# Optimization experiments

Hardware: AMD Instinct MI355X
Metric: run time of the kernel (lower is better)

## Reference

```python
import jax, jax.numpy as jnp
import numpy as np

C0 = 32          # cs[0] == cs[1] with planes=[32,32,...], cr=1.0
CIN = 4
EPS = 1e-5

# ---------- host-side coordinate hashing (mirrors F.sphash / F.sphashquery) ----------

def _enc(c):
    # unique int64 code per (x,y,z); +2 shift keeps offset-adjusted coords positive
    return (c[:, 0] + 2).astype(np.int64) + (c[:, 1] + 2).astype(np.int64) * 1024 \
        + (c[:, 2] + 2).astype(np.int64) * 1024 * 1024

def _lookup(sorted_codes, q):
    pos = np.searchsorted(sorted_codes, q)
    pos = np.minimum(pos, len(sorted_codes) - 1)
    return np.where(sorted_codes[pos] == q, pos, -1).astype(np.int32)

def _offsets(r):
    return np.array([[i, j, k] for i in r for j in r for k in r], np.int64)


def setup_inputs() -> dict:
    rng = np.random.default_rng(0)
    N0 = 400000
    pts = rng.integers(0, [400, 400, 40], size=(600000, 3)).astype(np.int64)
    codes = _enc(pts)
    codes_u, idx = np.unique(codes, return_index=True)
    assert len(codes_u) >= N0
    coords0, codes0 = pts[idx][:N0], codes_u[:N0]   # sorted by hash code

    off27, off8 = _offsets([-1, 0, 1]), _offsets([0, 1])
    # ks=3 stride=1 kernel map at level 0: nbr0[k, i] = index of coords0[i]+off27[k] (or -1)
    nbr0 = np.stack([_lookup(codes0, _enc(coords0 + o)) for o in off27])

    # stride-2 downsample coords (level 1)
    c1all = coords0 // 2
    codes1_u, i1 = np.unique(_enc(c1all), return_index=True)
    coords1 = c1all[i1]
    # ks=2 stride=2 kernel map: output voxel gathers inputs at 2*out + {0,1}^3
    down1 = np.stack([_lookup(codes0, _enc(coords1 * 2 + o)) for o in off8])
    # ks=3 stride=1 kernel map at level 1
    nbr1 = np.stack([_lookup(codes1_u, _enc(coords1 + o)) for o in off27])

    key = jax.random.key(0)
    ks = jax.random.split(key, 10)

    def w(k, K, ci, co):
        return jax.random.normal(k, (K, ci, co), jnp.float32) * (1.0 / np.sqrt(K * ci))

    return {
        "voxel_features": jax.random.normal(ks[0], (N0, CIN), jnp.float32),
        "W_stem1": w(ks[1], 27, CIN, C0),
        "W_stem2": w(ks[2], 27, C0, C0),
        "W_down":  w(ks[3], 8,  C0, C0),
        "W_r1a":   w(ks[4], 27, C0, C0),
        "W_r1b":   w(ks[5], 27, C0, C0),
        "W_r2a":   w(ks[6], 27, C0, C0),
        "W_r2b":   w(ks[7], 27, C0, C0),
        "gammas": jnp.ones((7, C0), jnp.float32),
        "betas":  jnp.zeros((7, C0), jnp.float32),
        "nbr0":  jnp.asarray(nbr0),
        "down1": jnp.asarray(down1),
        "nbr1":  jnp.asarray(nbr1),
    }


# ---------- sparse conv: gather-GEMM-scatter per kernel offset ----------

def _spconv(feat, nbr, W):
    # feat [N, Ci], nbr [K, M] (-1 = no neighbor), W [K, Ci, Co] -> out [M, Co]
    def step(acc, kw):
        idx, Wk = kw
        g = jnp.where((idx >= 0)[:, None], feat[jnp.maximum(idx, 0)], 0.0)
        return acc + g @ Wk, None
    acc0 = jnp.zeros((nbr.shape[1], W.shape[-1]), feat.dtype)
    out, _ = jax.lax.scan(step, acc0, (nbr, W))
    return out


def _bn(x, g, b):
    # BatchNorm1d, training-mode statistics (biased var), gamma/beta affine
    mu = x.mean(0)
    var = x.var(0)
    return (x - mu) * jax.lax.rsqrt(var + EPS) * g + b


def _cbr(x, nbr, W, g, b):
    return jax.nn.relu(_bn(_spconv(x, nbr, W), g, b))


def reference(voxel_features, W_stem1, W_stem2, W_down, W_r1a, W_r1b, W_r2a, W_r2b,
              gammas, betas, nbr0, down1, nbr1):
    g, b = gammas, betas
    # stem: two ks=3 sparse convs + BN + ReLU at level 0
    x = _cbr(voxel_features, nbr0, W_stem1, g[0], b[0])
    x = _cbr(x, nbr0, W_stem2, g[1], b[1])
    # stage1: BasicConvolutionBlock (ks=2, stride=2) + 2 ResidualBlocks at level 1
    x1 = _cbr(x, down1, W_down, g[2], b[2])
    h = _cbr(x1, nbr1, W_r1a, g[3], b[3])
    h = _bn(_spconv(h, nbr1, W_r1b), g[4], b[4])
    x1 = jax.nn.relu(h + x1)          # downsample == Identity (inc == outc, stride 1)
    h = _cbr(x1, nbr1, W_r2a, g[5], b[5])
    h = _bn(_spconv(h, nbr1, W_r2b), g[6], b[6])
    return jax.nn.relu(h + x1)
```

## Files before the change

kernel.cpp:

```cpp
#include <hip/hip_runtime.h>

#define EPS 1e-5f

typedef __attribute__((ext_vector_type(8))) short short8;
typedef __attribute__((ext_vector_type(4))) float floatx4;
typedef __attribute__((ext_vector_type(8))) unsigned short ushort8;
typedef __attribute__((ext_vector_type(4))) unsigned short ushortv4;

#define O_S1  0
#define O_S2  4096
#define O_DN  (O_S2 + 27648)
#define O_R1A (O_DN + 8192)
#define O_R1B (O_R1A + 27648)
#define O_R2A (O_R1B + 27648)
#define O_R2B (O_R2A + 27648)
#define WP_TOTAL (O_R2B + 27648)

__device__ __forceinline__ unsigned short f2bf(float f) {
    union { float f; unsigned u; } x; x.f = f;
    unsigned r = x.u + 0x7fffu + ((x.u >> 16) & 1u);
    return (unsigned short)(r >> 16);
}
__device__ __forceinline__ float bf2f(unsigned short b) {
    union { unsigned u; float f; } x; x.u = ((unsigned)b) << 16;
    return x.f;
}

__device__ __forceinline__ int xcd_swizzle(int nb) {
    int b = (int)blockIdx.x;
    int q = nb >> 3, r = nb & 7;
    int x = b & 7, i = b >> 3;
    return x * q + (x < r ? x : r) + i;
}

__device__ __forceinline__ short8 gath(const unsigned short* __restrict__ x,
                                       int ii, int q) {
    short8 z = {};
    return (ii >= 0) ? *(const short8*)(x + (size_t)ii * 32 + q * 8) : z;
}

__device__ __forceinline__ void pack_w_one(
    const float* __restrict__ W, unsigned short* __restrict__ out, int t)
{
    int lane = t & 63;
    int h = (t >> 6) & 1;
    int k = t >> 7;
    int m = lane & 15, q = lane >> 4;
    ushort8 v;
#pragma unroll
    for (int j = 0; j < 8; ++j)
        v[j] = f2bf(W[((size_t)k * 32 + q * 8 + j) * 32 + h * 16 + m]);
    *(ushort8*)(out + (size_t)t * 8) = v;
}

__global__ __launch_bounds__(256) void prep_kernel(
    const float* __restrict__ vf,
    const float* __restrict__ Ws1, const float* __restrict__ Ws2,
    const float* __restrict__ Wd,  const float* __restrict__ Wr1a,
    const float* __restrict__ Wr1b, const float* __restrict__ Wr2a,
    const float* __restrict__ Wr2b,
    unsigned short* __restrict__ xb, unsigned short* __restrict__ wp, int N0)
{
    int t = blockIdx.x * 256 + threadIdx.x;
    if (t < N0) {
        float4 v = *(const float4*)(vf + (size_t)t * 4);
        ushortv4 r = {f2bf(v.x), f2bf(v.y), f2bf(v.z), f2bf(v.w)};
        *(ushortv4*)(xb + (size_t)t * 4) = r;
        return;
    }
    t -= N0;
    if (t < 512) {
        int lane = t & 63;
        int h = (t >> 6) & 1;
        int c = t >> 7;
        int m = lane & 15, q = lane >> 4;
        ushort8 v;
#pragma unroll
        for (int j = 0; j < 8; ++j) {
            int kdim = c * 32 + q * 8 + j;
            int tap = kdim >> 2, ci = kdim & 3;
            v[j] = (tap < 27) ? f2bf(Ws1[((size_t)tap * 4 + ci) * 32 + h * 16 + m]) : 0;
        }
        *(ushort8*)(wp + O_S1 + (size_t)t * 8) = v;
        return;
    }
    t -= 512;
    if (t < 27 * 128) { pack_w_one(Ws2,  wp + O_S2,  t); return; }
    t -= 27 * 128;
    if (t < 8 * 128)  { pack_w_one(Wd,   wp + O_DN,  t); return; }
    t -= 8 * 128;
    if (t < 27 * 128) { pack_w_one(Wr1a, wp + O_R1A, t); return; }
    t -= 27 * 128;
    if (t < 27 * 128) { pack_w_one(Wr1b, wp + O_R1B, t); return; }
    t -= 27 * 128;
    if (t < 27 * 128) { pack_w_one(Wr2a, wp + O_R2A, t); return; }
    t -= 27 * 128;
    if (t < 27 * 128) { pack_w_one(Wr2b, wp + O_R2B, t); return; }
}

__device__ __forceinline__ void conv_epilogue2(
    floatx4 acc00, floatx4 acc01, floatx4 acc10, floatx4 acc11,
    unsigned short* __restrict__ y, float* __restrict__ part,
    int rowbase, int lb, int N, float* sm)
{
    const int lane = threadIdx.x & 63;
    const int m = lane & 15, q = lane >> 4;

    if (threadIdx.x < 64) sm[threadIdx.x] = 0.f;
    __syncthreads();

#pragma unroll
    for (int r = 0; r < 4; ++r) {
        int ra = rowbase + q * 4 + r;
        int rb = ra + 16;
        if (ra < N) {
            y[(size_t)ra * 32 + m]      = f2bf(acc00[r]);
            y[(size_t)ra * 32 + 16 + m] = f2bf(acc01[r]);
        }
        if (rb < N) {
            y[(size_t)rb * 32 + m]      = f2bf(acc10[r]);
            y[(size_t)rb * 32 + 16 + m] = f2bf(acc11[r]);
        }
    }

    float s0 = 0.f, q0 = 0.f, s1 = 0.f, q1 = 0.f;
#pragma unroll
    for (int r = 0; r < 4; ++r) {
        s0 += acc00[r] + acc10[r];
        q0 += acc00[r] * acc00[r] + acc10[r] * acc10[r];
        s1 += acc01[r] + acc11[r];
        q1 += acc01[r] * acc01[r] + acc11[r] * acc11[r];
    }
    s0 += __shfl_down(s0, 32); s0 += __shfl_down(s0, 16);
    q0 += __shfl_down(q0, 32); q0 += __shfl_down(q0, 16);
    s1 += __shfl_down(s1, 32); s1 += __shfl_down(s1, 16);
    q1 += __shfl_down(q1, 32); q1 += __shfl_down(q1, 16);
    if (lane < 16) {
        atomicAdd(&sm[m],      s0);
        atomicAdd(&sm[32 + m], q0);
        atomicAdd(&sm[16 + m],      s1);
        atomicAdd(&sm[48 + m], q1);
    }
    __syncthreads();
    if (threadIdx.x < 64)
        part[(size_t)lb * 64 + threadIdx.x] = sm[threadIdx.x];
}

#define MFMA_BF16 __builtin_amdgcn_mfma_f32_16x16x32_bf16
template <int K>
__global__ __launch_bounds__(256) void conv_mfma_kernel(
    const unsigned short* __restrict__ x,
    const int* __restrict__ nbr,
    const unsigned short* __restrict__ Wp,
    unsigned short* __restrict__ y,
    float* __restrict__ part, int N)
{
    __shared__ float sm[64];
    const int nb = (N + 255) / 256;
    const int lb = xcd_swizzle(nb);
    const int lane = threadIdx.x & 63;
    const int wave = threadIdx.x >> 6;
    const int m = lane & 15, q = lane >> 4;
    const int rowbase = lb * 256 + wave * 64;
    const int r0 = rowbase + m, r1 = r0 + 16, r2 = r0 + 32, r3 = r0 + 48;
    const bool v0 = r0 < N, v1 = r1 < N, v2 = r2 < N, v3 = r3 < N;

    floatx4 c00 = {0.f, 0.f, 0.f, 0.f};
    floatx4 c01 = c00, c10 = c00, c11 = c00;
    floatx4 c20 = c00, c21 = c00, c30 = c00, c31 = c00;

#define IDX(k, rr, vv) ((vv) ? nbr[(size_t)(k) * N + (rr)] : -1)

    int p0 = IDX(0, r0, v0), p1 = IDX(0, r1, v1), p2 = IDX(0, r2, v2), p3 = IDX(0, r3, v3);
    short8 a0 = gath(x, p0, q), a1 = gath(x, p1, q), a2 = gath(x, p2, q), a3 = gath(x, p3, q);
    int j0 = -1, j1 = -1, j2 = -1, j3 = -1;
    if (K > 1) { j0 = IDX(1, r0, v0); j1 = IDX(1, r1, v1); j2 = IDX(1, r2, v2); j3 = IDX(1, r3, v3); }

    for (int k = 0; k < K; ++k) {
        int n0 = -1, n1 = -1, n2 = -1, n3 = -1;
        if (k + 2 < K) {
            n0 = IDX(k + 2, r0, v0); n1 = IDX(k + 2, r1, v1);
            n2 = IDX(k + 2, r2, v2); n3 = IDX(k + 2, r3, v3);
        }
        short8 t0 = {}, t1 = {}, t2 = {}, t3 = {};
        if (k + 1 < K) {
            t0 = gath(x, j0, q); t1 = gath(x, j1, q);
            t2 = gath(x, j2, q); t3 = gath(x, j3, q);
        }
        const short8* wk = (const short8*)(Wp + (size_t)k * 1024);
        short8 b0 = wk[lane];
        short8 b1 = wk[64 + lane];
        c00 = MFMA_BF16(a0, b0, c00, 0, 0, 0);
        c01 = MFMA_BF16(a0, b1, c01, 0, 0, 0);
        c10 = MFMA_BF16(a1, b0, c10, 0, 0, 0);
        c11 = MFMA_BF16(a1, b1, c11, 0, 0, 0);
        c20 = MFMA_BF16(a2, b0, c20, 0, 0, 0);
        c21 = MFMA_BF16(a2, b1, c21, 0, 0, 0);
        c30 = MFMA_BF16(a3, b0, c30, 0, 0, 0);
        c31 = MFMA_BF16(a3, b1, c31, 0, 0, 0);
        a0 = t0; a1 = t1; a2 = t2; a3 = t3;
        j0 = n0; j1 = n1; j2 = n2; j3 = n3;
    }
#undef IDX

    if (threadIdx.x < 64) sm[threadIdx.x] = 0.f;
    __syncthreads();

#define STORE2(cA, cB, tb)                                        \
    _Pragma("unroll")                                             \
    for (int r = 0; r < 4; ++r) {                                 \
        int ra = rowbase + (tb) * 16 + q * 4 + r;                 \
        if (ra < N) {                                             \
            y[(size_t)ra * 32 + m]      = f2bf(cA[r]);            \
            y[(size_t)ra * 32 + 16 + m] = f2bf(cB[r]);            \
        }                                                         \
    }
    STORE2(c00, c01, 0) STORE2(c10, c11, 1) STORE2(c20, c21, 2) STORE2(c30, c31, 3)
#undef STORE2

    float s0 = 0.f, q0 = 0.f, s1 = 0.f, q1 = 0.f;
#pragma unroll
    for (int r = 0; r < 4; ++r) {
        s0 += c00[r] + c10[r] + c20[r] + c30[r];
        q0 += c00[r] * c00[r] + c10[r] * c10[r] + c20[r] * c20[r] + c30[r] * c30[r];
        s1 += c01[r] + c11[r] + c21[r] + c31[r];
        q1 += c01[r] * c01[r] + c11[r] * c11[r] + c21[r] * c21[r] + c31[r] * c31[r];
    }
    s0 += __shfl_down(s0, 32); s0 += __shfl_down(s0, 16);
    q0 += __shfl_down(q0, 32); q0 += __shfl_down(q0, 16);
    s1 += __shfl_down(s1, 32); s1 += __shfl_down(s1, 16);
    q1 += __shfl_down(q1, 32); q1 += __shfl_down(q1, 16);
    if (lane < 16) {
        atomicAdd(&sm[m],      s0);
        atomicAdd(&sm[32 + m], q0);
        atomicAdd(&sm[16 + m],      s1);
        atomicAdd(&sm[48 + m], q1);
    }
    __syncthreads();
    if (threadIdx.x < 64)
        part[(size_t)lb * 64 + threadIdx.x] = sm[threadIdx.x];
}

__global__ __launch_bounds__(256) void conv_stem1_mfma(
    const unsigned short* __restrict__ xb,
    const int* __restrict__ nbr,
    const unsigned short* __restrict__ Wp,
    unsigned short* __restrict__ y,
    float* __restrict__ part, int N)
{
    __shared__ float sm[64];
    const int nb = (N + 127) / 128;
    const int lb = xcd_swizzle(nb);
    const int lane = threadIdx.x & 63;
    const int wave = threadIdx.x >> 6;
    const int m = lane & 15, q = lane >> 4;
    const int rowbase = lb * 128 + wave * 32;
    const int row0 = rowbase + m;
    const int row1 = rowbase + 16 + m;

    floatx4 acc00 = {0.f, 0.f, 0.f, 0.f};
    floatx4 acc01 = acc00, acc10 = acc00, acc11 = acc00;

#pragma unroll
    for (int c = 0; c < 4; ++c) {
        const int t0 = c * 8 + q * 2, t1 = t0 + 1;
        short8 a0 = {}, a1 = {};
        {
            int ia = (t0 < 27 && row0 < N) ? nbr[(size_t)t0 * N + row0] : -1;
            int ib = (t1 < 27 && row0 < N) ? nbr[(size_t)t1 * N + row0] : -1;
            ushortv4 ga = {}, gb = {};
            if (ia >= 0) ga = *(const ushortv4*)(xb + (size_t)ia * 4);
            if (ib >= 0) gb = *(const ushortv4*)(xb + (size_t)ib * 4);
            a0[0] = (short)ga[0]; a0[1] = (short)ga[1];
            a0[2] = (short)ga[2]; a0[3] = (short)ga[3];
            a0[4] = (short)gb[0]; a0[5] = (short)gb[1];
            a0[6] = (short)gb[2]; a0[7] = (short)gb[3];
        }
        {
            int ia = (t0 < 27 && row1 < N) ? nbr[(size_t)t0 * N + row1] : -1;
            int ib = (t1 < 27 && row1 < N) ? nbr[(size_t)t1 * N + row1] : -1;
            ushortv4 ga = {}, gb = {};
            if (ia >= 0) ga = *(const ushortv4*)(xb + (size_t)ia * 4);
            if (ib >= 0) gb = *(const ushortv4*)(xb + (size_t)ib * 4);
            a1[0] = (short)ga[0]; a1[1] = (short)ga[1];
            a1[2] = (short)ga[2]; a1[3] = (short)ga[3];
            a1[4] = (short)gb[0]; a1[5] = (short)gb[1];
            a1[6] = (short)gb[2]; a1[7] = (short)gb[3];
        }
        const short8* wk = (const short8*)Wp;
        short8 b0 = wk[(c * 2 + 0) * 64 + lane];
        short8 b1 = wk[(c * 2 + 1) * 64 + lane];
        acc00 = MFMA_BF16(a0, b0, acc00, 0, 0, 0);
        acc01 = MFMA_BF16(a0, b1, acc01, 0, 0, 0);
        acc10 = MFMA_BF16(a1, b0, acc10, 0, 0, 0);
        acc11 = MFMA_BF16(a1, b1, acc11, 0, 0, 0);
    }

    conv_epilogue2(acc00, acc01, acc10, acc11, y, part, rowbase, lb, N, sm);
}

__global__ __launch_bounds__(256) void reduce_stats_kernel(
    const float* __restrict__ part, float* __restrict__ stats, int nb)
{
    __shared__ float sm[256];
    int t = threadIdx.x;
    int c = t & 63, g = t >> 6;
    float s = 0.f;
    for (int b = blockIdx.x * 4 + g; b < nb; b += 256)
        s += part[(size_t)b * 64 + c];
    sm[t] = s;
    __syncthreads();
    if (t < 64)
        atomicAdd(&stats[t], sm[t] + sm[64 + t] + sm[128 + t] + sm[192 + t]);
}

template <bool OUT_F32, bool HAS_RES>
__global__ __launch_bounds__(256) void bn_relu_kernel(
    const unsigned short* __restrict__ y, const float* __restrict__ stats,
    const float* __restrict__ gamma, const float* __restrict__ beta,
    const unsigned short* __restrict__ resid, void* __restrict__ outp, int N)
{
    int t = blockIdx.x * 256 + threadIdx.x;
    if (t >= N) return;
    float inv_n = 1.0f / (float)N;
    const ushort8* yr = (const ushort8*)(y + (size_t)t * 32);

#pragma unroll
    for (int c = 0; c < 4; ++c) {
        ushort8 v = yr[c];
        ushort8 rv = {};
        if (HAS_RES) rv = ((const ushort8*)(resid + (size_t)t * 32))[c];
        float f0, f1, f2, f3, f4, f5, f6, f7;
#define BNJ(fj, j)                                                        \
        {                                                                 \
            int co = c * 8 + (j);                                         \
            float mu = stats[co] * inv_n;                                 \
            float var = stats[32 + co] * inv_n - mu * mu;                 \
            float sc = rsqrtf(var + EPS) * gamma[co];                     \
            fj = (bf2f(v[j]) - mu) * sc + beta[co];                       \
            if (HAS_RES) fj += bf2f(rv[j]);                               \
            fj = fmaxf(fj, 0.0f);                                         \
        }
        BNJ(f0, 0) BNJ(f1, 1) BNJ(f2, 2) BNJ(f3, 3)
        BNJ(f4, 4) BNJ(f5, 5) BNJ(f6, 6) BNJ(f7, 7)
#undef BNJ
        if (OUT_F32) {
            float* ob = (float*)outp + (size_t)t * 32 + c * 8;
            floatx4 u0 = {f0, f1, f2, f3}, u1 = {f4, f5, f6, f7};
            *(floatx4*)(ob) = u0;
            *(floatx4*)(ob + 4) = u1;
        } else {
            ushort8 o;
            o[0] = f2bf(f0); o[1] = f2bf(f1); o[2] = f2bf(f2); o[3] = f2bf(f3);
            o[4] = f2bf(f4); o[5] = f2bf(f5); o[6] = f2bf(f6); o[7] = f2bf(f7);
            ((ushort8*)((unsigned short*)outp + (size_t)t * 32))[c] = o;
        }
    }
}

extern "C" void kernel_launch(void* const* d_in, const int* in_sizes, int n_in,
                              void* d_out, int out_size, void* d_ws, size_t ws_size,
                              hipStream_t stream)
{
    const float* vf   = (const float*)d_in[0];
    const float* Ws1  = (const float*)d_in[1];
    const float* Ws2  = (const float*)d_in[2];
    const float* Wd   = (const float*)d_in[3];
    const float* Wr1a = (const float*)d_in[4];
    const float* Wr1b = (const float*)d_in[5];
    const float* Wr2a = (const float*)d_in[6];
    const float* Wr2b = (const float*)d_in[7];
    const float* gam  = (const float*)d_in[8];
    const float* bet  = (const float*)d_in[9];
    const int* nbr0   = (const int*)d_in[10];
    const int* down1  = (const int*)d_in[11];
    const int* nbr1   = (const int*)d_in[12];

    int N0 = in_sizes[0] / 4;
    int N1 = in_sizes[11] / 8;

    unsigned short* yraw = (unsigned short*)d_ws;
    unsigned short* actA = yraw + (size_t)N0 * 32;
    unsigned short* actB = actA + (size_t)N0 * 32;
    unsigned short* xb   = actB + (size_t)N0 * 32;
    unsigned short* wp   = xb + (size_t)N0 * 4;
    float* part  = (float*)(wp + WP_TOTAL);
    float* stats = part + (size_t)3200 * 64;

    hipMemsetAsync(stats, 0, 7 * 64 * sizeof(float), stream);

    auto g1 = [](int n) { return dim3((unsigned)((n + 255) / 256)); };
    auto gm = [](int n) { return dim3((unsigned)((n + 255) / 256)); };
    auto gs = [](int n) { return dim3((unsigned)((n + 127) / 128)); };
    int nbs1 = (N0 + 127) / 128;
    int nb0 = (N0 + 255) / 256;
    int nb1 = (N1 + 255) / 256;

    int prep_threads = N0 + 512 + 128 * (27 * 5 + 8);
    prep_kernel<<<g1(prep_threads), 256, 0, stream>>>(
        vf, Ws1, Ws2, Wd, Wr1a, Wr1b, Wr2a, Wr2b, xb, wp, N0);

    conv_stem1_mfma<<<gs(N0), 256, 0, stream>>>(xb, nbr0, wp + O_S1, yraw, part, N0);
    reduce_stats_kernel<<<64, 256, 0, stream>>>(part, stats + 0 * 64, nbs1);
    bn_relu_kernel<false, false><<<g1(N0), 256, 0, stream>>>(yraw, stats + 0 * 64, gam + 0, bet + 0, nullptr, actA, N0);
    conv_mfma_kernel<27><<<gm(N0), 256, 0, stream>>>(actA, nbr0, wp + O_S2, yraw, part, N0);
    reduce_stats_kernel<<<64, 256, 0, stream>>>(part, stats + 1 * 64, nb0);
    bn_relu_kernel<false, false><<<g1(N0), 256, 0, stream>>>(yraw, stats + 1 * 64, gam + 32, bet + 32, nullptr, actB, N0);
    conv_mfma_kernel<8><<<gm(N1), 256, 0, stream>>>(actB, down1, wp + O_DN, yraw, part, N1);
    reduce_stats_kernel<<<64, 256, 0, stream>>>(part, stats + 2 * 64, nb1);
    bn_relu_kernel<false, false><<<g1(N1), 256, 0, stream>>>(yraw, stats + 2 * 64, gam + 64, bet + 64, nullptr, actA, N1);
    conv_mfma_kernel<27><<<gm(N1), 256, 0, stream>>>(actA, nbr1, wp + O_R1A, yraw, part, N1);
    reduce_stats_kernel<<<64, 256, 0, stream>>>(part, stats + 3 * 64, nb1);
    bn_relu_kernel<false, false><<<g1(N1), 256, 0, stream>>>(yraw, stats + 3 * 64, gam + 96, bet + 96, nullptr, actB, N1);
    conv_mfma_kernel<27><<<gm(N1), 256, 0, stream>>>(actB, nbr1, wp + O_R1B, yraw, part, N1);
    reduce_stats_kernel<<<64, 256, 0, stream>>>(part, stats + 4 * 64, nb1);
    bn_relu_kernel<false, true><<<g1(N1), 256, 0, stream>>>(yraw, stats + 4 * 64, gam + 128, bet + 128, actA, actB, N1);
    conv_mfma_kernel<27><<<gm(N1), 256, 0, stream>>>(actB, nbr1, wp + O_R2A, yraw, part, N1);
    reduce_stats_kernel<<<64, 256, 0, stream>>>(part, stats + 5 * 64, nb1);
    bn_relu_kernel<false, false><<<g1(N1), 256, 0, stream>>>(yraw, stats + 5 * 64, gam + 160, bet + 160, nullptr, actA, N1);
    conv_mfma_kernel<27><<<gm(N1), 256, 0, stream>>>(actA, nbr1, wp + O_R2B, yraw, part, N1);
    reduce_stats_kernel<<<64, 256, 0, stream>>>(part, stats + 6 * 64, nb1);
    bn_relu_kernel<true, true><<<g1(N1), 256, 0, stream>>>(yraw, stats + 6 * 64, gam + 192, bet + 192, actB, d_out, N1);
}
```

Baseline: 634.7 us.

## Stage contiguous neighbor-row windows in LDS for sparse conv gathers

The conv kernel now processes taps in groups that share the same y/z offsets. For each group the block computes the min/max neighbor index, copies that contiguous span of feature rows into shared memory, and gathers operands from LDS. This relies on the hash-sorted layout keeping neighbors close in index. If the span is larger than the window, it falls back to direct global gathers. The change drops the previous software-pipelined prefetch, adds several block-wide barriers and reductions per group, and uses a large LDS buffer that may lower occupancy.

```diff
diff --git a/kernel.cpp b/kernel.cpp
--- a/kernel.cpp
+++ b/kernel.cpp
@@ -1,6 +1,7 @@
 #include <hip/hip_runtime.h>
 
 #define EPS 1e-5f
+#define WROWS 480
 
 typedef __attribute__((ext_vector_type(8))) short short8;
 typedef __attribute__((ext_vector_type(4))) float floatx4;
@@ -147,6 +148,7 @@
 }
 
 #define MFMA_BF16 __builtin_amdgcn_mfma_f32_16x16x32_bf16
+
 template <int K>
 __global__ __launch_bounds__(256) void conv_mfma_kernel(
     const unsigned short* __restrict__ x,
@@ -155,7 +157,14 @@
     unsigned short* __restrict__ y,
     float* __restrict__ part, int N)
 {
+    constexpr int XV     = (K == 27) ? 3 : 2;
+    constexpr int GROUPS = (K == 27) ? 9 : 4;
+    constexpr int S      = GROUPS;
+
+    __shared__ __align__(16) unsigned short win[WROWS * 40];
     __shared__ float sm[64];
+    __shared__ int wmm[2];
+
     const int nb = (N + 255) / 256;
     const int lb = xcd_swizzle(nb);
     const int lane = threadIdx.x & 63;
@@ -170,38 +179,100 @@
     floatx4 c20 = c00, c21 = c00, c30 = c00, c31 = c00;
 
 #define IDX(k, rr, vv) ((vv) ? nbr[(size_t)(k) * N + (rr)] : -1)
-
-    int p0 = IDX(0, r0, v0), p1 = IDX(0, r1, v1), p2 = IDX(0, r2, v2), p3 = IDX(0, r3, v3);
-    short8 a0 = gath(x, p0, q), a1 = gath(x, p1, q), a2 = gath(x, p2, q), a3 = gath(x, p3, q);
-    int j0 = -1, j1 = -1, j2 = -1, j3 = -1;
-    if (K > 1) { j0 = IDX(1, r0, v0); j1 = IDX(1, r1, v1); j2 = IDX(1, r2, v2); j3 = IDX(1, r3, v3); }
-
-    for (int k = 0; k < K; ++k) {
-        int n0 = -1, n1 = -1, n2 = -1, n3 = -1;
-        if (k + 2 < K) {
-            n0 = IDX(k + 2, r0, v0); n1 = IDX(k + 2, r1, v1);
-            n2 = IDX(k + 2, r2, v2); n3 = IDX(k + 2, r3, v3);
-        }
-        short8 t0 = {}, t1 = {}, t2 = {}, t3 = {};
-        if (k + 1 < K) {
-            t0 = gath(x, j0, q); t1 = gath(x, j1, q);
-            t2 = gath(x, j2, q); t3 = gath(x, j3, q);
-        }
-        const short8* wk = (const short8*)(Wp + (size_t)k * 1024);
-        short8 b0 = wk[lane];
-        short8 b1 = wk[64 + lane];
-        c00 = MFMA_BF16(a0, b0, c00, 0, 0, 0);
-        c01 = MFMA_BF16(a0, b1, c01, 0, 0, 0);
-        c10 = MFMA_BF16(a1, b0, c10, 0, 0, 0);
-        c11 = MFMA_BF16(a1, b1, c11, 0, 0, 0);
-        c20 = MFMA_BF16(a2, b0, c20, 0, 0, 0);
-        c21 = MFMA_BF16(a2, b1, c21, 0, 0, 0);
-        c30 = MFMA_BF16(a3, b0, c30, 0, 0, 0);
-        c31 = MFMA_BF16(a3, b1, c31, 0, 0, 0);
-        a0 = t0; a1 = t1; a2 = t2; a3 = t3;
-        j0 = n0; j1 = n1; j2 = n2; j3 = n3;
+#define LG(ii) ({ short8 z_ = {}; \
+    (ii) >= 0 ? *(const short8*)(&win[((ii) - wmin) * 40 + q * 8]) : z_; })
+#define PROC_TAP(A0, A1, A2, A3, tap)                         \
+    {                                                         \
+        const short8* wk = (const short8*)(Wp + (size_t)(tap) * 1024); \
+        short8 b0 = wk[lane];                                 \
+        short8 b1 = wk[64 + lane];                            \
+        c00 = MFMA_BF16(A0, b0, c00, 0, 0, 0);                \
+        c01 = MFMA_BF16(A0, b1, c01, 0, 0, 0);                \
+        c10 = MFMA_BF16(A1, b0, c10, 0, 0, 0);                \
+        c11 = MFMA_BF16(A1, b1, c11, 0, 0, 0);                \
+        c20 = MFMA_BF16(A2, b0, c20, 0, 0, 0);                \
+        c21 = MFMA_BF16(A2, b1, c21, 0, 0, 0);                \
+        c30 = MFMA_BF16(A3, b0, c30, 0, 0, 0);                \
+        c31 = MFMA_BF16(A3, b1, c31, 0, 0, 0);                \
+    }
+
+    for (int g = 0; g < GROUPS; ++g) {
+        if (threadIdx.x == 0) { wmm[0] = 0x7fffffff; wmm[1] = -1; }
+        __syncthreads();
+
+        int ia0 = IDX(g, r0, v0), ia1 = IDX(g, r1, v1);
+        int ia2 = IDX(g, r2, v2), ia3 = IDX(g, r3, v3);
+        int ib0 = IDX(g + S, r0, v0), ib1 = IDX(g + S, r1, v1);
+        int ib2 = IDX(g + S, r2, v2), ib3 = IDX(g + S, r3, v3);
+        int ic0 = -1, ic1 = -1, ic2 = -1, ic3 = -1;
+        if (XV == 3) {
+            ic0 = IDX(g + 2 * S, r0, v0); ic1 = IDX(g + 2 * S, r1, v1);
+            ic2 = IDX(g + 2 * S, r2, v2); ic3 = IDX(g + 2 * S, r3, v3);
+        }
+
+#define MN(a) ((a) < 0 ? 0x7fffffff : (a))
+        int lmin = min(min(min(MN(ia0), MN(ia1)), min(MN(ia2), MN(ia3))),
+                       min(min(MN(ib0), MN(ib1)), min(MN(ib2), MN(ib3))));
+        int lmax = max(max(max(ia0, ia1), max(ia2, ia3)),
+                       max(max(ib0, ib1), max(ib2, ib3)));
+        if (XV == 3) {
+            lmin = min(lmin, min(min(MN(ic0), MN(ic1)), min(MN(ic2), MN(ic3))));
+            lmax = max(lmax, max(max(ic0, ic1), max(ic2, ic3)));
+        }
+#undef MN
+#pragma unroll
+        for (int off = 32; off >= 1; off >>= 1) {
+            lmin = min(lmin, __shfl_down(lmin, off));
+            lmax = max(lmax, __shfl_down(lmax, off));
+        }
+        if (lane == 0) { atomicMin(&wmm[0], lmin); atomicMax(&wmm[1], lmax); }
+        __syncthreads();
+
+        const int wmin = wmm[0];
+        const int wspan = wmm[1] - wmin + 1;
+        const bool any = (wmm[1] >= 0);
+
+        if (any && wspan <= WROWS) {
+            const short8* src = (const short8*)(x + (size_t)wmin * 32);
+            for (int c = threadIdx.x; c < wspan * 4; c += 256) {
+                int rr = c >> 2, hh = c & 3;
+                *(short8*)&win[rr * 40 + hh * 8] = src[c];
+            }
+            __syncthreads();
+            {
+                short8 a0 = LG(ia0), a1 = LG(ia1), a2 = LG(ia2), a3 = LG(ia3);
+                PROC_TAP(a0, a1, a2, a3, g)
+            }
+            {
+                short8 a0 = LG(ib0), a1 = LG(ib1), a2 = LG(ib2), a3 = LG(ib3);
+                PROC_TAP(a0, a1, a2, a3, g + S)
+            }
+            if (XV == 3) {
+                short8 a0 = LG(ic0), a1 = LG(ic1), a2 = LG(ic2), a3 = LG(ic3);
+                PROC_TAP(a0, a1, a2, a3, g + 2 * S)
+            }
+        } else if (any) {
+            {
+                short8 a0 = gath(x, ia0, q), a1 = gath(x, ia1, q);
+                short8 a2 = gath(x, ia2, q), a3 = gath(x, ia3, q);
+                PROC_TAP(a0, a1, a2, a3, g)
+            }
+            {
+                short8 a0 = gath(x, ib0, q), a1 = gath(x, ib1, q);
+                short8 a2 = gath(x, ib2, q), a3 = gath(x, ib3, q);
+                PROC_TAP(a0, a1, a2, a3, g + S)
+            }
+            if (XV == 3) {
+                short8 a0 = gath(x, ic0, q), a1 = gath(x, ic1, q);
+                short8 a2 = gath(x, ic2, q), a3 = gath(x, ic3, q);
+                PROC_TAP(a0, a1, a2, a3, g + 2 * S)
+            }
+        }
+        __syncthreads();
     }
 #undef IDX
+#undef LG
+#undef PROC_TAP
 
     if (threadIdx.x < 64) sm[threadIdx.x] = 0.f;
     __syncthreads();
```

After: 716.5 us. 12.9% more time.
